# Optimization experiments

Measured on AMD Instinct MI355X. Metric: run time of the kernel, lower is better.

## Reference

```python
import jax, jax.numpy as jnp
import numpy as np

TWO_PI = 2.0 * np.pi
EPS = 1e-6

# mixture packed layout along last axis (7): [weight, px, py, cxx, cxy, cyx, cyy]

def unpack(m):
    w = m[..., 0]
    p = m[..., 1:3]
    C = m[..., 3:7].reshape(m.shape[:-1] + (2, 2))
    return w, p, C

def pack(w, p, C):
    return jnp.concatenate([w[..., None], p, C.reshape(C.shape[:-2] + (4,))], axis=-1)

def det2(C):
    return C[..., 0, 0] * C[..., 1, 1] - C[..., 0, 1] * C[..., 1, 0]

def inv2(C):
    d = det2(C)[..., None, None]
    adj = jnp.stack([
        jnp.stack([C[..., 1, 1], -C[..., 0, 1]], axis=-1),
        jnp.stack([-C[..., 1, 0], C[..., 0, 0]], axis=-1)], axis=-2)
    return adj / d

def component_integrals(w, C):
    # integral of an amplitude-parameterized 2D gaussian: w * 2*pi * sqrt(det C)
    return w * TWO_PI * jnp.sqrt(jnp.maximum(det2(C), EPS))

def gm_convolve(data, kernel):
    # data [B,Li,Nd,7], kernel [Lo,Li,Nk,7] -> [B,Lo,Li*Nd*Nk,7]
    wd, pd, Cd = unpack(data)
    wk, pk, Ck = unpack(kernel)
    dd = det2(Cd)[:, None, :, :, None]              # [B,1,Li,Nd,1]
    dk = det2(Ck)[None, :, :, None, :]              # [1,Lo,Li,1,Nk]
    Cs = Cd[:, None, :, :, None, :, :] + Ck[None, :, :, None, :, :, :]  # [B,Lo,Li,Nd,Nk,2,2]
    ps = pd[:, None, :, :, None, :] + pk[None, :, :, None, :, :]        # [B,Lo,Li,Nd,Nk,2]
    # amplitude of convolved gaussian so that integrals multiply
    ws = (wd[:, None, :, :, None] * wk[None, :, :, None, :]
          * TWO_PI * jnp.sqrt(dd * dk / jnp.maximum(det2(Cs), EPS)))
    m = pack(ws, ps, Cs)
    B, Lo = m.shape[0], m.shape[1]
    return m.reshape(B, Lo, -1, 7)

def eval_at_centers(w, p, C):
    # value of the whole mixture at each component center; [.., N]
    Ci = inv2(C)                                        # [..,N,2,2]
    diff = p[..., :, None, :] - p[..., None, :, :]      # [..,K,N,2]
    md = jnp.einsum('...kni,...nij,...knj->...kn', diff, Ci, diff)
    return jnp.einsum('...n,...kn->...k', w, jnp.exp(-0.5 * md))

def relu_fit(m, bias, n_out):
    # fitting-based ReLU: rescale each component so the mixture matches
    # relu(m(x)+b) at the centers, then keep the n_out largest components
    w, p, C = unpack(m)
    v = eval_at_centers(w, p, C) + bias[None, :, None]  # [B,L,N]
    scale = jax.nn.relu(v) / (jnp.abs(v) + EPS)
    w2 = w * scale
    _, idx = jax.lax.top_k(jnp.abs(w2), n_out)          # [B,L,n_out]
    w_s = jnp.take_along_axis(w2, idx, axis=-1)
    p_s = jnp.take_along_axis(p, jnp.broadcast_to(idx[..., None], idx.shape + (2,)), axis=-2)
    Cf = C.reshape(C.shape[:-2] + (4,))
    C_s = jnp.take_along_axis(Cf, jnp.broadcast_to(idx[..., None], idx.shape + (4,)), axis=-2)
    return pack(w_s, p_s, C_s.reshape(C_s.shape[:-1] + (2, 2)))

def batchnorm(m, per_gaussian):
    w, p, C = unpack(m)
    tot = jnp.sum(jnp.abs(component_integrals(w, C)), axis=-1, keepdims=True)  # [B,L,1]
    if not per_gaussian:
        tot = jnp.mean(tot, axis=0, keepdims=True)      # batch statistic per channel
    return pack(w / (tot + EPS), p, C)

def integrate(m):
    w, _, C = unpack(m)
    return jnp.sum(component_integrals(w, C), axis=-1)  # [B,L]

def forward(in_x, kernel1, kernel2, kernel3, bias1, bias2, bias3):
    x = batchnorm(in_x, per_gaussian=True)   # bn0
    x = gm_convolve(x, kernel1)              # [B,5,320,7]
    x = relu_fit(x, bias1, 25)
    x = batchnorm(x, per_gaussian=False)
    x = gm_convolve(x, kernel2)              # [B,6,625,7]
    x = relu_fit(x, bias2, 12)
    x = batchnorm(x, per_gaussian=False)
    x = gm_convolve(x, kernel3)              # [B,10,360,7]
    x = relu_fit(x, bias3, 5)
    x = batchnorm(x, per_gaussian=False)
    out = jax.nn.log_softmax(integrate(x), axis=1)
    return out.reshape(-1, 10)

def _make_kernel(key, lo, li, nk, weight_sd, position_range, covariance_range):
    kw, kp = jax.random.split(key)
    w = jax.random.normal(kw, (lo, li, nk)) * weight_sd
    p = jax.random.uniform(kp, (lo, li, nk, 2), minval=-position_range, maxval=position_range)
    C = jnp.broadcast_to(covariance_range * jnp.eye(2), (lo, li, nk, 2, 2))
    return pack(w, p, C).astype(jnp.float32)

def setup_inputs() -> dict:
    key = jax.random.key(0)
    k = jax.random.split(key, 8)
    B, NIN, NK = 32, 64, 5
    w = jax.random.uniform(k[0], (B, 1, NIN), minval=0.05, maxval=1.0)
    p = jax.random.uniform(k[1], (B, 1, NIN, 2), minval=-14.0, maxval=14.0)
    cdiag = jax.random.uniform(k[2], (B, 1, NIN, 2), minval=0.5, maxval=2.0)
    C = jnp.zeros((B, 1, NIN, 2, 2)).at[..., 0, 0].set(cdiag[..., 0]).at[..., 1, 1].set(cdiag[..., 1])
    in_x = pack(w, p, C).astype(jnp.float32)
    return {
        'in_x': in_x,
        'kernel1': _make_kernel(k[3], 5, 1, NK, 0.4, 2.0, 0.5),
        'kernel2': _make_kernel(k[4], 6, 5, NK, 0.04, 4.0, 2.0),
        'kernel3': _make_kernel(k[5], 10, 6, NK, 0.025, 8.0, 4.0),
        'bias1': jnp.zeros((5,), jnp.float32),
        'bias2': jnp.zeros((6,), jnp.float32),
        'bias3': jnp.zeros((10,), jnp.float32),
    }

def reference(in_x, kernel1, kernel2, kernel3, bias1, bias2, bias3):
    return forward(in_x, kernel1, kernel2, kernel3, bias1, bias2, bias3)
```

## Files before the change

### kernel.cpp

```cpp
#include <hip/hip_runtime.h>

#define TWO_PI_F 6.283185307179586f
#define EPS_F 1e-6f
#define LOG2E_F 1.4426950408889634f
#define BATCH 32

#if __has_builtin(__builtin_amdgcn_exp2f)
#define EXP2F(x) __builtin_amdgcn_exp2f(x)
#else
#define EXP2F(x) exp2f(x)
#endif

typedef float v2f __attribute__((ext_vector_type(2)));

__device__ __forceinline__ float sane(float x) {
    return ((__float_as_uint(x) & 0x7f800000u) == 0x7f800000u) ? 0.f : x;
}

__global__ __launch_bounds__(1024) void layer_unified(
    const float* __restrict__ in_x,
    const float* __restrict__ prev_sel,
    const float* __restrict__ prev_tot,
    const float* __restrict__ kern,
    const float* __restrict__ bias,
    float* __restrict__ out_sel,
    float* __restrict__ out_tot,
    const int LO, const int LI, const int ND, const int NK,
    const int NCOMP, const int KOUT,
    const int TPGL,
    const int G, const int CHUNK, const int CHUNKP,
    const int KUSE, const int first)
{
    constexpr int KP = 5, NT = 1024, NPAIR = 2;
    constexpr int M_NCOMP = 625, M_NCOMP4 = 628, M_NPADT = 8*80 + 4;
    constexpr int M_ACC   = 5120;
    struct StageT {
        float4 d_c[125];
        float4 k_c[25];
        float  d_w[125], d_px[125], d_py[125];
        float  k_w[25],  k_px[25],  k_py[25];
    };
    constexpr size_t ACCB = (size_t)M_ACC * sizeof(float);
    constexpr size_t UB   = sizeof(StageT) > ACCB ? sizeof(StageT) : ACCB;
    __shared__ __align__(16) unsigned char u_smem[UB];
    StageT& st    = *reinterpret_cast<StageT*>(u_smem);
    float* accbuf = reinterpret_cast<float*>(u_smem);

    __shared__ float2 cPos[M_NCOMP];
    __shared__ float4 nP[M_NPADT];
    __shared__ float4 nQ[M_NPADT];
    __shared__ float4 cC[M_NCOMP];
    __shared__ float  w2s[M_NCOMP];
    __shared__ __align__(16) float a2s[M_NCOMP4];
    __shared__ __align__(16) float scr[64];
    __shared__ float  selint[32];
    __shared__ float  dscale[8];
    __shared__ float  ptot[BATCH*5];

    const int b   = blockIdx.x / LO;
    const int lo  = blockIdx.x - b*LO;
    const int tid = threadIdx.x;
    const int tpg = 1 << TPGL;
    const int g   = tid >> TPGL;
    const int kt  = tid & (tpg - 1);
    const bool active = (kt < KUSE);
    const int NQn = (NCOMP + 3) >> 2;
    const int NCOMP4 = NQn << 2;
    const int NPADT = G*CHUNKP + 4;

    if (first) {
        if (tid < ND) {
            const float* s = in_x + (size_t)(b*ND + tid)*7;
            const float w  = sane(s[0]);
            const float c0 = sane(s[3]), c1 = sane(s[4]), c2 = sane(s[5]), c3 = sane(s[6]);
            st.d_w[tid] = w; st.d_px[tid] = sane(s[1]); st.d_py[tid] = sane(s[2]);
            st.d_c[tid] = make_float4(c0, c1, c2, c3);
            const float det = c0*c3 - c1*c2;
            scr[tid] = sane(fabsf(w) * TWO_PI_F * sqrtf(fmaxf(det, EPS_F)));
        }
        __syncthreads();
        if (tid == 0) {
            float s = 0.f;
            const float4* s4 = (const float4*)scr;
            const int nq = ND >> 2;
            for (int i = 0; i < nq; ++i) {
                const float4 v = s4[i];
                s += v.x; s += v.y; s += v.z; s += v.w;
            }
            dscale[0] = 1.f / (s + EPS_F);
        }
        __syncthreads();
        if (tid < ND) st.d_w[tid] = sane(st.d_w[tid] * dscale[0]);
    } else {
        for (int i = tid; i < BATCH*LI; i += NT) ptot[i] = prev_tot[i];
        __syncthreads();
        if (tid < LI) {
            float s = 0.f;
            #pragma unroll 1
            for (int bb = 0; bb < BATCH; ++bb) s += ptot[bb*LI + tid];
            dscale[tid] = 1.f / (s / (float)BATCH + EPS_F);
        }
        __syncthreads();
        if (tid < LI*ND) {
            const int li = tid / ND;
            const float* s = prev_sel + (size_t)(b*LI*ND + tid)*7;
            st.d_w[tid]  = sane(s[0] * dscale[li]);
            st.d_px[tid] = s[1]; st.d_py[tid] = s[2];
            st.d_c[tid]  = make_float4(s[3], s[4], s[5], s[6]);
        }
    }
    if (tid < LI*NK) {
        const float* s = kern + (size_t)(lo*LI*NK + tid)*7;
        st.k_w[tid]  = sane(s[0]);
        st.k_px[tid] = sane(s[1]); st.k_py[tid] = sane(s[2]);
        st.k_c[tid]  = make_float4(sane(s[3]), sane(s[4]), sane(s[5]), sane(s[6]));
    }
    for (int r = tid; r < NPADT; r += NT) {
        const int gg = r / CHUNKP;
        const int ss = r - gg*CHUNKP;
        const bool valid = (gg < G) && (ss < CHUNK) && (gg*CHUNK + ss < NCOMP);
        if (!valid) {
            nP[r] = make_float4(0.f, 0.f, 0.f, 0.f);
            nQ[r] = make_float4(0.f, 0.f, 0.f, 0.f);
        }
    }
    __syncthreads();

    if (tid < NCOMP) {
        const int li = tid / (ND*NK);
        const int r  = tid - li*(ND*NK);
        const int nd = r / NK, nk = r - (r/NK)*NK;
        const int di = li*ND + nd, ki = li*NK + nk;
        const float4 dc = st.d_c[di], kc = st.k_c[ki];
        const float c0 = dc.x + kc.x, c1 = dc.y + kc.y, c2 = dc.z + kc.z, c3 = dc.w + kc.w;
        const float dd = dc.x*dc.w - dc.y*dc.z;
        const float dk = kc.x*kc.w - kc.y*kc.z;
        const float ds = c0*c3 - c1*c2;
        const float w  = sane(st.d_w[di]*st.k_w[ki]*TWO_PI_F*sqrtf(fmaxf(dd*dk, 0.f) / fmaxf(ds, EPS_F)));
        const float px = sane(st.d_px[di] + st.k_px[ki]);
        const float py = sane(st.d_py[di] + st.k_py[ki]);
        const float inv = -0.5f * LOG2E_F / ds;
        const float a   = sane(c3*inv);
        const float bb  = sane(-(c1 + c2)*inv);
        const float cc  = sane(c0*inv);
        const float dd2 = sane(-(2.f*a*px + bb*py));
        const float ee  = sane(-(2.f*cc*py + bb*px));
        const float ff  = sane((a*px + bb*py)*px + cc*py*py);
        const int grp = tid / CHUNK;
        const int row = grp*CHUNKP + (tid - grp*CHUNK);
        cPos[tid] = make_float2(px, py);
        nP[row]   = make_float4(a, bb, cc, dd2);
        nQ[row]   = make_float4(ee, ff, w, 0.f);
        cC[tid]   = make_float4(sane(c0), sane(c1), sane(c2), sane(c3));
    }
    __syncthreads();

    v2f kxP[NPAIR], kyP[NPAIR], kx2P[NPAIR], ky2P[NPAIR], kxyP[NPAIR], accP[NPAIR];
    float kxS = 0.f, kyS = 0.f, kx2S = 0.f, ky2S = 0.f, kxyS = 0.f, accS = 0.f;
    #pragma unroll
    for (int p = 0; p < NPAIR; ++p) {
        float x0 = 0.f, y0 = 0.f, x1 = 0.f, y1 = 0.f;
        if (active) {
            const float2 p0 = cPos[kt + (2*p    )*KUSE];
            const float2 p1 = cPos[kt + (2*p + 1)*KUSE];
            x0 = p0.x; y0 = p0.y; x1 = p1.x; y1 = p1.y;
        }
        v2f kx; kx.x = x0; kx.y = x1;
        v2f ky; ky.x = y0; ky.y = y1;
        kxP[p] = kx; kyP[p] = ky;
        kx2P[p] = kx*kx; ky2P[p] = ky*ky; kxyP[p] = kx*ky;
        v2f z; z.x = 0.f; z.y = 0.f; accP[p] = z;
    }
    {
        if (active) { const float2 pz = cPos[kt + (KP-1)*KUSE]; kxS = pz.x; kyS = pz.y; }
        kx2S = kxS*kxS; ky2S = kyS*kyS; kxyS = kxS*kyS;
    }
    {
        const float4* __restrict__ bP = &nP[g*CHUNKP];
        const float4* __restrict__ bQ = &nQ[g*CHUNKP];
        float4 P0 = bP[0], Q0 = bQ[0];
        float4 P1 = bP[1], Q1 = bQ[1];
        float4 P2 = bP[2], Q2 = bQ[2];
        float4 P3 = bP[3], Q3 = bQ[3];
        int nr = 4;
        const int quads = CHUNKP >> 2;

#define PHB_STEP(PP,QQ)                                                       \
        {   const float4 Pn_ = bP[nr], Qn_ = bQ[nr]; ++nr;                    \
            v2f Pa; Pa.x = PP.x; Pa.y = PP.x;                                 \
            v2f Pb; Pb.x = PP.y; Pb.y = PP.y;                                 \
            v2f Pc; Pc.x = PP.z; Pc.y = PP.z;                                 \
            v2f Pd; Pd.x = PP.w; Pd.y = PP.w;                                 \
            v2f Qe; Qe.x = QQ.x; Qe.y = QQ.x;                                 \
            v2f Qf; Qf.x = QQ.y; Qf.y = QQ.y;                                 \
            v2f Qw; Qw.x = QQ.z; Qw.y = QQ.z;                                 \
            _Pragma("unroll")                                                 \
            for (int p = 0; p < NPAIR; ++p) {                                 \
                const v2f md = __builtin_elementwise_fma(Pa, kx2P[p],         \
                               __builtin_elementwise_fma(Pb, kxyP[p],         \
                               __builtin_elementwise_fma(Pc, ky2P[p],         \
                               __builtin_elementwise_fma(Pd, kxP[p],          \
                               __builtin_elementwise_fma(Qe, kyP[p], Qf)))));  \
                v2f ex; ex.x = EXP2F(md.x); ex.y = EXP2F(md.y);               \
                accP[p] = __builtin_elementwise_fma(Qw, ex, accP[p]);         \
            }                                                                 \
            {                                                                 \
                const float md = fmaf(PP.x, kx2S,                             \
                                 fmaf(PP.y, kxyS,                             \
                                 fmaf(PP.z, ky2S,                             \
                                 fmaf(PP.w, kxS,                              \
                                 fmaf(QQ.x, kyS, QQ.y)))));                   \
                accS = fmaf(QQ.z, EXP2F(md), accS);                           \
            }                                                                 \
            PP = Pn_; QQ = Qn_; }

        #pragma unroll 1
        for (int i4 = 0; i4 < quads; ++i4) {
            PHB_STEP(P0, Q0)
            PHB_STEP(P1, Q1)
            PHB_STEP(P2, Q2)
            PHB_STEP(P3, Q3)
        }
#undef PHB_STEP
    }
    float acc[KP];
    #pragma unroll
    for (int p = 0; p < NPAIR; ++p) { acc[2*p] = accP[p].x; acc[2*p+1] = accP[p].y; }
    acc[KP-1] = accS;

    if (active) {
        #pragma unroll
        for (int j = 0; j < KP; ++j) accbuf[(g*tpg + kt)*KP + j] = acc[j];
    }
    __syncthreads();

    const float bi = bias[lo];
    if (tid < NCOMP) {
        const int j2  = tid / KUSE;
        const int kt2 = tid - j2*KUSE;
        float s = accbuf[kt2*KP + j2];
        #pragma unroll 1
        for (int g2 = 1; g2 < G; ++g2) s += accbuf[(g2*tpg + kt2)*KP + j2];
        const float v  = s + bi;
        const float sc = fmaxf(v, 0.f) / (fabsf(v) + EPS_F);
        const int grp = tid / CHUNK;
        const int row = grp*CHUNKP + (tid - grp*CHUNK);
        const float ww = sane(nQ[row].z * sc);
        w2s[tid] = ww;
        a2s[tid] = fabsf(ww);
    }
    for (int i = NCOMP + tid - (tid < NCOMP ? tid : tid); false;) {}
    if (tid >= NCOMP && tid < NCOMP4) a2s[tid] = -1.f;
    __syncthreads();

    const int CQ = (NQn + G - 1) / G;
    int rank[KP];
    float myv[KP];
    #pragma unroll
    for (int j = 0; j < KP; ++j) rank[j] = 0;
    if (active) {
        #pragma unroll
        for (int j = 0; j < KP; ++j) myv[j] = a2s[kt + j*KUSE];
        const int q0 = g*CQ;
        const int q1 = (q0 + CQ < NQn) ? (q0 + CQ) : NQn;
        #pragma unroll 1
        for (int q = q0; q < q1; ++q) {
            const float4 v4 = ((const float4*)a2s)[q];
            #pragma unroll
            for (int c = 0; c < 4; ++c) {
                const float vj = (c == 0) ? v4.x : (c == 1) ? v4.y : (c == 2) ? v4.z : v4.w;
                const int   jj = 4*q + c;
                #pragma unroll
                for (int j = 0; j < KP; ++j) {
                    const int myk = kt + j*KUSE;
                    rank[j] += (vj > myv[j] || (vj == myv[j] && jj < myk)) ? 1 : 0;
                }
            }
        }
        #pragma unroll
        for (int j = 0; j < KP; ++j) accbuf[(g*tpg + kt)*KP + j] = (float)rank[j];
    }
    __syncthreads();

    if (tid < NCOMP) {
        const int j2  = tid / KUSE;
        const int kt2 = tid - j2*KUSE;
        int r = 0;
        #pragma unroll 1
        for (int g2 = 0; g2 < G; ++g2) r += (int)accbuf[(g2*tpg + kt2)*KP + j2];
        if (r < KOUT) {
            const float2 p = cPos[tid];
            const float4 c = cC[tid];
            const float ww = w2s[tid];
            float* dst = out_sel + (size_t)((b*LO + lo)*KOUT + r)*7;
            dst[0] = ww; dst[1] = p.x; dst[2] = p.y;
            dst[3] = c.x; dst[4] = c.y; dst[5] = c.z; dst[6] = c.w;
            const float det = c.x*c.w - c.y*c.z;
            selint[r] = sane(fabsf(ww) * TWO_PI_F * sqrtf(fmaxf(det, EPS_F)));
        }
    }
    __syncthreads();
    if (tid == 0) {
        float s = 0.f;
        #pragma unroll 1
        for (int i = 0; i < KOUT; ++i) s += selint[i];
        out_tot[b*LO + lo] = s;
    }
}

template<int LO, int LI, int ND, int NK, int NCOMP, int KOUT,
         int KP, int TPG, int G, bool FIRST>
__global__ __launch_bounds__(TPG*G) void layer_kernel(
    const float* __restrict__ in_x,
    const float* __restrict__ prev_sel,
    const float* __restrict__ prev_tot,
    const float* __restrict__ kern,
    const float* __restrict__ bias,
    float* __restrict__ out_sel,
    float* __restrict__ out_tot)
{
    constexpr int KUSE   = NCOMP / KP;
    static_assert(KUSE * KP == NCOMP, "exact k tiling required");
    constexpr int NT     = TPG * G;
    static_assert(NT >= NCOMP, "one k per thread in reduce/select phases");
    constexpr int CHUNK  = (NCOMP + G - 1) / G;
    constexpr int NPADT  = G*CHUNK + 4;
    constexpr int NCOMP4 = (NCOMP + 3) & ~3;
    constexpr int NQn    = NCOMP4 / 4;
    constexpr int NPAIR  = KP / 2;
    constexpr int PPAD   = NPAIR > 0 ? NPAIR : 1;
    constexpr bool ODD   = (KP & 1) != 0;

    const int b   = blockIdx.x / LO;
    const int lo  = blockIdx.x % LO;
    const int tid = threadIdx.x;
    const int g   = tid / TPG;
    const int kt  = tid % TPG;
    const bool active = (kt < KUSE);

    struct StageT {
        float4 d_c[LI*ND];
        float4 k_c[LI*NK];
        float  d_w[LI*ND], d_px[LI*ND], d_py[LI*ND];
        float  k_w[LI*NK], k_px[LI*NK], k_py[LI*NK];
    };
    constexpr size_t ACCB = (size_t)G*TPG*KP * sizeof(float);
    constexpr size_t UB   = sizeof(StageT) > ACCB ? sizeof(StageT) : ACCB;
    __shared__ __align__(16) unsigned char u_smem[UB];
    StageT& st    = *reinterpret_cast<StageT*>(u_smem);
    float* accbuf = reinterpret_cast<float*>(u_smem);

    __shared__ float2 cPos[NCOMP];
    __shared__ float4 nP[NPADT];
    __shared__ float4 nQ[NPADT];
    __shared__ float4 cC[NCOMP];
    __shared__ float  w2s[NCOMP];
    __shared__ __align__(16) float a2s[NCOMP4];
    __shared__ __align__(16) float scr[64];
    __shared__ float  selint[32];
    __shared__ float  dscale[LI];
    __shared__ float  ptot[FIRST ? 1 : BATCH*LI];

    if constexpr (FIRST) {
        if (tid < ND) {
            const float* s = in_x + (size_t)(b*ND + tid)*7;
            const float w  = sane(s[0]);
            const float c0 = sane(s[3]), c1 = sane(s[4]), c2 = sane(s[5]), c3 = sane(s[6]);
            st.d_w[tid] = w; st.d_px[tid] = sane(s[1]); st.d_py[tid] = sane(s[2]);
            st.d_c[tid] = make_float4(c0, c1, c2, c3);
            const float det = c0*c3 - c1*c2;
            scr[tid] = sane(fabsf(w) * TWO_PI_F * sqrtf(fmaxf(det, EPS_F)));
        }
        __syncthreads();
        if (tid == 0) {
            float s = 0.f;
            const float4* s4 = (const float4*)scr;
            for (int i = 0; i < 16; ++i) {
                const float4 v = s4[i];
                s += v.x; s += v.y; s += v.z; s += v.w;
            }
            dscale[0] = 1.f / (s + EPS_F);
        }
        __syncthreads();
        if (tid < ND) st.d_w[tid] = sane(st.d_w[tid] * dscale[0]);
    } else {
        for (int i = tid; i < BATCH*LI; i += NT) ptot[i] = prev_tot[i];
        __syncthreads();
        if (tid < LI) {
            float s = 0.f;
            #pragma unroll 1
            for (int bb = 0; bb < BATCH; ++bb) s += ptot[bb*LI + tid];
            dscale[tid] = 1.f / (s / (float)BATCH + EPS_F);
        }
        __syncthreads();
        if (tid < LI*ND) {
            const int li = tid / ND;
            const float* s = prev_sel + (size_t)(b*LI*ND + tid)*7;
            st.d_w[tid]  = sane(s[0] * dscale[li]);
            st.d_px[tid] = s[1]; st.d_py[tid] = s[2];
            st.d_c[tid]  = make_float4(s[3], s[4], s[5], s[6]);
        }
    }
    if (tid < LI*NK) {
        const float* s = kern + (size_t)(lo*LI*NK + tid)*7;
        st.k_w[tid]  = sane(s[0]);
        st.k_px[tid] = sane(s[1]); st.k_py[tid] = sane(s[2]);
        st.k_c[tid]  = make_float4(sane(s[3]), sane(s[4]), sane(s[5]), sane(s[6]));
    }
    __syncthreads();

    if (tid < NCOMP) {
        const int li = tid / (ND*NK);
        const int r  = tid % (ND*NK);
        const int nd = r / NK, nk = r % NK;
        const int di = li*ND + nd, ki = li*NK + nk;
        const float4 dc = st.d_c[di], kc = st.k_c[ki];
        const float c0 = dc.x + kc.x, c1 = dc.y + kc.y, c2 = dc.z + kc.z, c3 = dc.w + kc.w;
        const float dd = dc.x*dc.w - dc.y*dc.z;
        const float dk = kc.x*kc.w - kc.y*kc.z;
        const float ds = c0*c3 - c1*c2;
        const float w  = sane(st.d_w[di]*st.k_w[ki]*TWO_PI_F*sqrtf(fmaxf(dd*dk, 0.f) / fmaxf(ds, EPS_F)));
        const float px = sane(st.d_px[di] + st.k_px[ki]);
        const float py = sane(st.d_py[di] + st.k_py[ki]);
        const float inv = -0.5f * LOG2E_F / ds;
        const float a   = sane(c3*inv);
        const float bb  = sane(-(c1 + c2)*inv);
        const float cc  = sane(c0*inv);
        const float dd2 = sane(-(2.f*a*px + bb*py));
        const float ee  = sane(-(2.f*cc*py + bb*px));
        const float ff  = sane((a*px + bb*py)*px + cc*py*py);
        cPos[tid] = make_float2(px, py);
        nP[tid]   = make_float4(a, bb, cc, dd2);
        nQ[tid]   = make_float4(ee, ff, w, 0.f);
        cC[tid]   = make_float4(sane(c0), sane(c1), sane(c2), sane(c3));
    }
    for (int i = NCOMP + tid; i < NPADT; i += NT) {
        nP[i] = make_float4(0.f, 0.f, 0.f, 0.f);
        nQ[i] = make_float4(0.f, 0.f, 0.f, 0.f);
    }
    __syncthreads();

    v2f kxP[PPAD], kyP[PPAD], kx2P[PPAD], ky2P[PPAD], kxyP[PPAD], accP[PPAD];
    float kxS = 0.f, kyS = 0.f, kx2S = 0.f, ky2S = 0.f, kxyS = 0.f, accS = 0.f;
    #pragma unroll
    for (int p = 0; p < NPAIR; ++p) {
        float x0 = 0.f, y0 = 0.f, x1 = 0.f, y1 = 0.f;
        if (active) {
            const float2 p0 = cPos[kt + (2*p    )*KUSE];
            const float2 p1 = cPos[kt + (2*p + 1)*KUSE];
            x0 = p0.x; y0 = p0.y; x1 = p1.x; y1 = p1.y;
        }
        v2f kx; kx.x = x0; kx.y = x1;
        v2f ky; ky.x = y0; ky.y = y1;
        kxP[p] = kx; kyP[p] = ky;
        kx2P[p] = kx*kx; ky2P[p] = ky*ky; kxyP[p] = kx*ky;
        v2f z; z.x = 0.f; z.y = 0.f; accP[p] = z;
    }
    if constexpr (ODD) {
        if (active) { const float2 pz = cPos[kt + (KP-1)*KUSE]; kxS = pz.x; kyS = pz.y; }
        kx2S = kxS*kxS; ky2S = kyS*kyS; kxyS = kxS*kyS;
    }
    {
        const int n0 = g*CHUNK;
        const float4* __restrict__ bP = &nP[n0];
        const float4* __restrict__ bQ = &nQ[n0];
        float4 P0 = bP[0], Q0 = bQ[0];
        float4 P1 = bP[1], Q1 = bQ[1];
        float4 P2 = bP[2], Q2 = bQ[2];
        float4 P3 = bP[3], Q3 = bQ[3];
        int nr = 4;

#define PHB_STEP(PP,QQ)                                                       \
        {   const float4 Pn_ = bP[nr], Qn_ = bQ[nr]; ++nr;                    \
            v2f Pa; Pa.x = PP.x; Pa.y = PP.x;                                 \
            v2f Pb; Pb.x = PP.y; Pb.y = PP.y;                                 \
            v2f Pc; Pc.x = PP.z; Pc.y = PP.z;                                 \
            v2f Pd; Pd.x = PP.w; Pd.y = PP.w;                                 \
            v2f Qe; Qe.x = QQ.x; Qe.y = QQ.x;                                 \
            v2f Qf; Qf.x = QQ.y; Qf.y = QQ.y;                                 \
            v2f Qw; Qw.x = QQ.z; Qw.y = QQ.z;                                 \
            _Pragma("unroll")                                                 \
            for (int p = 0; p < NPAIR; ++p) {                                 \
                const v2f md = __builtin_elementwise_fma(Pa, kx2P[p],         \
                               __builtin_elementwise_fma(Pb, kxyP[p],         \
                               __builtin_elementwise_fma(Pc, ky2P[p],         \
                               __builtin_elementwise_fma(Pd, kxP[p],          \
                               __builtin_elementwise_fma(Qe, kyP[p], Qf)))));  \
                v2f ex; ex.x = EXP2F(md.x); ex.y = EXP2F(md.y);               \
                accP[p] = __builtin_elementwise_fma(Qw, ex, accP[p]);         \
            }                                                                 \
            if constexpr (ODD) {                                              \
                const float md = fmaf(PP.x, kx2S,                             \
                                 fmaf(PP.y, kxyS,                             \
                                 fmaf(PP.z, ky2S,                             \
                                 fmaf(PP.w, kxS,                              \
                                 fmaf(QQ.x, kyS, QQ.y)))));                   \
                accS = fmaf(QQ.z, EXP2F(md), accS);                           \
            }                                                                 \
            PP = Pn_; QQ = Qn_; }

        #pragma unroll 1
        for (int i4 = 0; i4 < CHUNK/4; ++i4) {
            PHB_STEP(P0, Q0)
            PHB_STEP(P1, Q1)
            PHB_STEP(P2, Q2)
            PHB_STEP(P3, Q3)
        }
        if constexpr ((CHUNK % 4) >= 1) PHB_STEP(P0, Q0)
        if constexpr ((CHUNK % 4) >= 2) PHB_STEP(P1, Q1)
        if constexpr ((CHUNK % 4) >= 3) PHB_STEP(P2, Q2)
#undef PHB_STEP
    }
    float acc[KP];
    #pragma unroll
    for (int p = 0; p < NPAIR; ++p) { acc[2*p] = accP[p].x; acc[2*p+1] = accP[p].y; }
    if constexpr (ODD) acc[KP-1] = accS;

    if (active) {
        #pragma unroll
        for (int j = 0; j < KP; ++j) accbuf[(g*TPG + kt)*KP + j] = acc[j];
    }
    __syncthreads();

    const float bi = bias[lo];
    if (tid < NCOMP) {
        const int kt2 = tid % KUSE;
        const int j2  = tid / KUSE;
        float s = accbuf[(kt2)*KP + j2];
        #pragma unroll
        for (int g2 = 1; g2 < G; ++g2) s += accbuf[(g2*TPG + kt2)*KP + j2];
        const float v  = s + bi;
        const float sc = fmaxf(v, 0.f) / (fabsf(v) + EPS_F);
        const float ww = sane(nQ[tid].z * sc);
        w2s[tid] = ww;
        a2s[tid] = fabsf(ww);
    }
    if constexpr (NCOMP4 > NCOMP) {
        if (tid >= NCOMP && tid < NCOMP4) a2s[tid] = -1.f;
    }
    __syncthreads();

    constexpr int CQ = (NQn + G - 1) / G;
    int rank[KP];
    float myv[KP];
    #pragma unroll
    for (int j = 0; j < KP; ++j) rank[j] = 0;
    if (active) {
        #pragma unroll
        for (int j = 0; j < KP; ++j) myv[j] = a2s[kt + j*KUSE];
        const int q0 = g*CQ;
        const int q1 = (q0 + CQ < NQn) ? (q0 + CQ) : NQn;
        for (int q = q0; q < q1; ++q) {
            const float4 v4 = ((const float4*)a2s)[q];
            #pragma unroll
            for (int c = 0; c < 4; ++c) {
                const float vj = (c == 0) ? v4.x : (c == 1) ? v4.y : (c == 2) ? v4.z : v4.w;
                const int   jj = 4*q + c;
                #pragma unroll
                for (int j = 0; j < KP; ++j) {
                    const int myk = kt + j*KUSE;
                    rank[j] += (vj > myv[j] || (vj == myv[j] && jj < myk)) ? 1 : 0;
                }
            }
        }
        #pragma unroll
        for (int j = 0; j < KP; ++j) accbuf[(g*TPG + kt)*KP + j] = (float)rank[j];
    }
    __syncthreads();

    if (tid < NCOMP) {
        const int kt2 = tid % KUSE;
// ... 26 lines not shown
    float* __restrict__ out)
{
    const int b = blockIdx.x;
    const int tid = threadIdx.x;
    __shared__ float scale3[10], integ[10], red2[2];
    if (tid < 10) {
        float s = 0.f;
        for (int bb = 0; bb < BATCH; ++bb) s += tot3[bb*10 + tid];
        scale3[tid] = 1.f / (s / (float)BATCH + EPS_F);
    }
    __syncthreads();
    if (tid < 10) {
        float s = 0.f;
        const float* base = sel3 + (size_t)((b*10 + tid)*5)*7;
        for (int kk = 0; kk < 5; ++kk) {
            const float* c = base + kk*7;
            const float det = c[3]*c[6] - c[4]*c[5];
            s += c[0] * scale3[tid] * TWO_PI_F * sqrtf(fmaxf(det, EPS_F));
        }
        integ[tid] = sane(s);
    }
    __syncthreads();
    if (tid == 0) {
        float m = -1e30f;
        for (int l = 0; l < 10; ++l) m = fmaxf(m, integ[l]);
        float ss = 0.f;
        for (int l = 0; l < 10; ++l) ss += __expf(integ[l] - m);
        red2[0] = m; red2[1] = logf(ss);
    }
    __syncthreads();
    if (tid < 10) out[b*10 + tid] = integ[tid] - red2[0] - red2[1];
}

extern "C" void kernel_launch(void* const* d_in, const int* in_sizes, int n_in,
                              void* d_out, int out_size, void* d_ws, size_t ws_size,
                              hipStream_t stream)
{
    const float* in_x = (const float*)d_in[0];
    const float* k1   = (const float*)d_in[1];
    const float* k2   = (const float*)d_in[2];
    const float* k3   = (const float*)d_in[3];
    const float* b1   = (const float*)d_in[4];
    const float* b2   = (const float*)d_in[5];
    const float* b3   = (const float*)d_in[6];
    float* out = (float*)d_out;

    float* ws = (float*)d_ws;
    float* sel1 = ws;
    float* tot1 = ws + 28000;
    float* sel2 = ws + 28160;
    float* tot2 = ws + 44288;
    float* sel3 = ws + 44480;
    float* tot3 = ws + 55680;

    layer_unified<<<BATCH*5, 1024, 0, stream>>>(
        in_x, nullptr, nullptr, k1, b1, sel1, tot1,
        5, 1, 64, 5, 320, 25, 6, 16, 20, 20, 64, 1);
    layer_unified<<<BATCH*6, 1024, 0, stream>>>(
        nullptr, sel1, tot1, k2, b2, sel2, tot2,
        6, 5, 25, 5, 625, 12, 7, 8, 79, 80, 125, 0);
    layer_kernel<10, 6, 12, 5, 360, 5, 6, 64, 12, false><<<BATCH*10, 768, 0, stream>>>(
        nullptr, sel2, tot2, k3, b3, sel3, tot3);
    final_kernel<<<BATCH, 64, 0, stream>>>(sel3, tot3, out);
}
```

Measured before the change: 148.3 us.

## Split layers 1-2 into separate evaluation and selection kernels via global scratch

```diff
diff --git a/kernel.cpp b/kernel.cpp
--- a/kernel.cpp
+++ b/kernel.cpp
@@ -17,347 +17,43 @@
     return ((__float_as_uint(x) & 0x7f800000u) == 0x7f800000u) ? 0.f : x;
 }
 
-__global__ __launch_bounds__(1024) void layer_unified(
+
+template<int LO, int LI, int ND, int NK, int NCOMP,
+         int KP, int TPG, int G, bool FIRST>
+__global__ __launch_bounds__(TPG*G) void layer_partA(
     const float* __restrict__ in_x,
     const float* __restrict__ prev_sel,
     const float* __restrict__ prev_tot,
     const float* __restrict__ kern,
-    const float* __restrict__ bias,
-    float* __restrict__ out_sel,
-    float* __restrict__ out_tot,
-    const int LO, const int LI, const int ND, const int NK,
-    const int NCOMP, const int KOUT,
-    const int TPGL,
-    const int G, const int CHUNK, const int CHUNKP,
-    const int KUSE, const int first)
-{
-    constexpr int KP = 5, NT = 1024, NPAIR = 2;
-    constexpr int M_NCOMP = 625, M_NCOMP4 = 628, M_NPADT = 8*80 + 4;
-    constexpr int M_ACC   = 5120;
-    struct StageT {
-        float4 d_c[125];
-        float4 k_c[25];
-        float  d_w[125], d_px[125], d_py[125];
-        float  k_w[25],  k_px[25],  k_py[25];
-    };
-    constexpr size_t ACCB = (size_t)M_ACC * sizeof(float);
-    constexpr size_t UB   = sizeof(StageT) > ACCB ? sizeof(StageT) : ACCB;
-    __shared__ __align__(16) unsigned char u_smem[UB];
-    StageT& st    = *reinterpret_cast<StageT*>(u_smem);
-    float* accbuf = reinterpret_cast<float*>(u_smem);
-
-    __shared__ float2 cPos[M_NCOMP];
-    __shared__ float4 nP[M_NPADT];
-    __shared__ float4 nQ[M_NPADT];
-    __shared__ float4 cC[M_NCOMP];
-    __shared__ float  w2s[M_NCOMP];
-    __shared__ __align__(16) float a2s[M_NCOMP4];
-    __shared__ __align__(16) float scr[64];
-    __shared__ float  selint[32];
-    __shared__ float  dscale[8];
-    __shared__ float  ptot[BATCH*5];
-
-    const int b   = blockIdx.x / LO;
-    const int lo  = blockIdx.x - b*LO;
-    const int tid = threadIdx.x;
-    const int tpg = 1 << TPGL;
-    const int g   = tid >> TPGL;
-    const int kt  = tid & (tpg - 1);
-    const bool active = (kt < KUSE);
-    const int NQn = (NCOMP + 3) >> 2;
-    const int NCOMP4 = NQn << 2;
-    const int NPADT = G*CHUNKP + 4;
-
-    if (first) {
-        if (tid < ND) {
-            const float* s = in_x + (size_t)(b*ND + tid)*7;
-            const float w  = sane(s[0]);
-            const float c0 = sane(s[3]), c1 = sane(s[4]), c2 = sane(s[5]), c3 = sane(s[6]);
-            st.d_w[tid] = w; st.d_px[tid] = sane(s[1]); st.d_py[tid] = sane(s[2]);
-            st.d_c[tid] = make_float4(c0, c1, c2, c3);
-            const float det = c0*c3 - c1*c2;
-            scr[tid] = sane(fabsf(w) * TWO_PI_F * sqrtf(fmaxf(det, EPS_F)));
-        }
-        __syncthreads();
-        if (tid == 0) {
-            float s = 0.f;
-            const float4* s4 = (const float4*)scr;
-            const int nq = ND >> 2;
-            for (int i = 0; i < nq; ++i) {
-                const float4 v = s4[i];
-                s += v.x; s += v.y; s += v.z; s += v.w;
-            }
-            dscale[0] = 1.f / (s + EPS_F);
-        }
-        __syncthreads();
-        if (tid < ND) st.d_w[tid] = sane(st.d_w[tid] * dscale[0]);
-    } else {
-        for (int i = tid; i < BATCH*LI; i += NT) ptot[i] = prev_tot[i];
-        __syncthreads();
-        if (tid < LI) {
-            float s = 0.f;
-            #pragma unroll 1
-            for (int bb = 0; bb < BATCH; ++bb) s += ptot[bb*LI + tid];
-            dscale[tid] = 1.f / (s / (float)BATCH + EPS_F);
-        }
-        __syncthreads();
-        if (tid < LI*ND) {
-            const int li = tid / ND;
-            const float* s = prev_sel + (size_t)(b*LI*ND + tid)*7;
-            st.d_w[tid]  = sane(s[0] * dscale[li]);
-            st.d_px[tid] = s[1]; st.d_py[tid] = s[2];
-            st.d_c[tid]  = make_float4(s[3], s[4], s[5], s[6]);
-        }
-    }
-    if (tid < LI*NK) {
-        const float* s = kern + (size_t)(lo*LI*NK + tid)*7;
-        st.k_w[tid]  = sane(s[0]);
-        st.k_px[tid] = sane(s[1]); st.k_py[tid] = sane(s[2]);
-        st.k_c[tid]  = make_float4(sane(s[3]), sane(s[4]), sane(s[5]), sane(s[6]));
-    }
-    for (int r = tid; r < NPADT; r += NT) {
-        const int gg = r / CHUNKP;
-        const int ss = r - gg*CHUNKP;
-        const bool valid = (gg < G) && (ss < CHUNK) && (gg*CHUNK + ss < NCOMP);
-        if (!valid) {
-            nP[r] = make_float4(0.f, 0.f, 0.f, 0.f);
-            nQ[r] = make_float4(0.f, 0.f, 0.f, 0.f);
-        }
-    }
-    __syncthreads();
-
-    if (tid < NCOMP) {
-        const int li = tid / (ND*NK);
-        const int r  = tid - li*(ND*NK);
-        const int nd = r / NK, nk = r - (r/NK)*NK;
-        const int di = li*ND + nd, ki = li*NK + nk;
-        const float4 dc = st.d_c[di], kc = st.k_c[ki];
-        const float c0 = dc.x + kc.x, c1 = dc.y + kc.y, c2 = dc.z + kc.z, c3 = dc.w + kc.w;
-        const float dd = dc.x*dc.w - dc.y*dc.z;
-        const float dk = kc.x*kc.w - kc.y*kc.z;
-        const float ds = c0*c3 - c1*c2;
-        const float w  = sane(st.d_w[di]*st.k_w[ki]*TWO_PI_F*sqrtf(fmaxf(dd*dk, 0.f) / fmaxf(ds, EPS_F)));
-        const float px = sane(st.d_px[di] + st.k_px[ki]);
-        const float py = sane(st.d_py[di] + st.k_py[ki]);
-        const float inv = -0.5f * LOG2E_F / ds;
-        const float a   = sane(c3*inv);
-        const float bb  = sane(-(c1 + c2)*inv);
-        const float cc  = sane(c0*inv);
-        const float dd2 = sane(-(2.f*a*px + bb*py));
-        const float ee  = sane(-(2.f*cc*py + bb*px));
-        const float ff  = sane((a*px + bb*py)*px + cc*py*py);
-        const int grp = tid / CHUNK;
-        const int row = grp*CHUNKP + (tid - grp*CHUNK);
-        cPos[tid] = make_float2(px, py);
-        nP[row]   = make_float4(a, bb, cc, dd2);
-        nQ[row]   = make_float4(ee, ff, w, 0.f);
-        cC[tid]   = make_float4(sane(c0), sane(c1), sane(c2), sane(c3));
-    }
-    __syncthreads();
-
-    v2f kxP[NPAIR], kyP[NPAIR], kx2P[NPAIR], ky2P[NPAIR], kxyP[NPAIR], accP[NPAIR];
-    float kxS = 0.f, kyS = 0.f, kx2S = 0.f, ky2S = 0.f, kxyS = 0.f, accS = 0.f;
-    #pragma unroll
-    for (int p = 0; p < NPAIR; ++p) {
-        float x0 = 0.f, y0 = 0.f, x1 = 0.f, y1 = 0.f;
-        if (active) {
-            const float2 p0 = cPos[kt + (2*p    )*KUSE];
-            const float2 p1 = cPos[kt + (2*p + 1)*KUSE];
-            x0 = p0.x; y0 = p0.y; x1 = p1.x; y1 = p1.y;
-        }
-        v2f kx; kx.x = x0; kx.y = x1;
-        v2f ky; ky.x = y0; ky.y = y1;
-        kxP[p] = kx; kyP[p] = ky;
-        kx2P[p] = kx*kx; ky2P[p] = ky*ky; kxyP[p] = kx*ky;
-        v2f z; z.x = 0.f; z.y = 0.f; accP[p] = z;
-    }
-    {
-        if (active) { const float2 pz = cPos[kt + (KP-1)*KUSE]; kxS = pz.x; kyS = pz.y; }
-        kx2S = kxS*kxS; ky2S = kyS*kyS; kxyS = kxS*kyS;
-    }
-    {
-        const float4* __restrict__ bP = &nP[g*CHUNKP];
-        const float4* __restrict__ bQ = &nQ[g*CHUNKP];
-        float4 P0 = bP[0], Q0 = bQ[0];
-        float4 P1 = bP[1], Q1 = bQ[1];
-        float4 P2 = bP[2], Q2 = bQ[2];
-        float4 P3 = bP[3], Q3 = bQ[3];
-        int nr = 4;
-        const int quads = CHUNKP >> 2;
-
-#define PHB_STEP(PP,QQ)                                                       \
-        {   const float4 Pn_ = bP[nr], Qn_ = bQ[nr]; ++nr;                    \
-            v2f Pa; Pa.x = PP.x; Pa.y = PP.x;                                 \
-            v2f Pb; Pb.x = PP.y; Pb.y = PP.y;                                 \
-            v2f Pc; Pc.x = PP.z; Pc.y = PP.z;                                 \
-            v2f Pd; Pd.x = PP.w; Pd.y = PP.w;                                 \
-            v2f Qe; Qe.x = QQ.x; Qe.y = QQ.x;                                 \
-            v2f Qf; Qf.x = QQ.y; Qf.y = QQ.y;                                 \
-            v2f Qw; Qw.x = QQ.z; Qw.y = QQ.z;                                 \
-            _Pragma("unroll")                                                 \
-            for (int p = 0; p < NPAIR; ++p) {                                 \
-                const v2f md = __builtin_elementwise_fma(Pa, kx2P[p],         \
-                               __builtin_elementwise_fma(Pb, kxyP[p],         \
-                               __builtin_elementwise_fma(Pc, ky2P[p],         \
-                               __builtin_elementwise_fma(Pd, kxP[p],          \
-                               __builtin_elementwise_fma(Qe, kyP[p], Qf)))));  \
-                v2f ex; ex.x = EXP2F(md.x); ex.y = EXP2F(md.y);               \
-                accP[p] = __builtin_elementwise_fma(Qw, ex, accP[p]);         \
-            }                                                                 \
-            {                                                                 \
-                const float md = fmaf(PP.x, kx2S,                             \
-                                 fmaf(PP.y, kxyS,                             \
-                                 fmaf(PP.z, ky2S,                             \
-                                 fmaf(PP.w, kxS,                              \
-                                 fmaf(QQ.x, kyS, QQ.y)))));                   \
-                accS = fmaf(QQ.z, EXP2F(md), accS);                           \
-            }                                                                 \
-            PP = Pn_; QQ = Qn_; }
-
-        #pragma unroll 1
-        for (int i4 = 0; i4 < quads; ++i4) {
-            PHB_STEP(P0, Q0)
-            PHB_STEP(P1, Q1)
-            PHB_STEP(P2, Q2)
-            PHB_STEP(P3, Q3)
-        }
-#undef PHB_STEP
-    }
-    float acc[KP];
-    #pragma unroll
-    for (int p = 0; p < NPAIR; ++p) { acc[2*p] = accP[p].x; acc[2*p+1] = accP[p].y; }
-    acc[KP-1] = accS;
-
-    if (active) {
-        #pragma unroll
-        for (int j = 0; j < KP; ++j) accbuf[(g*tpg + kt)*KP + j] = acc[j];
-    }
-    __syncthreads();
-
-    const float bi = bias[lo];
-    if (tid < NCOMP) {
-        const int j2  = tid / KUSE;
-        const int kt2 = tid - j2*KUSE;
-        float s = accbuf[kt2*KP + j2];
-        #pragma unroll 1
-        for (int g2 = 1; g2 < G; ++g2) s += accbuf[(g2*tpg + kt2)*KP + j2];
-        const float v  = s + bi;
-        const float sc = fmaxf(v, 0.f) / (fabsf(v) + EPS_F);
-        const int grp = tid / CHUNK;
-        const int row = grp*CHUNKP + (tid - grp*CHUNK);
-        const float ww = sane(nQ[row].z * sc);
-        w2s[tid] = ww;
-        a2s[tid] = fabsf(ww);
-    }
-    for (int i = NCOMP + tid - (tid < NCOMP ? tid : tid); false;) {}
-    if (tid >= NCOMP && tid < NCOMP4) a2s[tid] = -1.f;
-    __syncthreads();
-
-    const int CQ = (NQn + G - 1) / G;
-    int rank[KP];
-    float myv[KP];
-    #pragma unroll
-    for (int j = 0; j < KP; ++j) rank[j] = 0;
-    if (active) {
-        #pragma unroll
-        for (int j = 0; j < KP; ++j) myv[j] = a2s[kt + j*KUSE];
-        const int q0 = g*CQ;
-        const int q1 = (q0 + CQ < NQn) ? (q0 + CQ) : NQn;
-        #pragma unroll 1
-        for (int q = q0; q < q1; ++q) {
-            const float4 v4 = ((const float4*)a2s)[q];
-            #pragma unroll
-            for (int c = 0; c < 4; ++c) {
-                const float vj = (c == 0) ? v4.x : (c == 1) ? v4.y : (c == 2) ? v4.z : v4.w;
-                const int   jj = 4*q + c;
-                #pragma unroll
-                for (int j = 0; j < KP; ++j) {
-                    const int myk = kt + j*KUSE;
-                    rank[j] += (vj > myv[j] || (vj == myv[j] && jj < myk)) ? 1 : 0;
-                }
-            }
-        }
-        #pragma unroll
-        for (int j = 0; j < KP; ++j) accbuf[(g*tpg + kt)*KP + j] = (float)rank[j];
-    }
-    __syncthreads();
-
-    if (tid < NCOMP) {
-        const int j2  = tid / KUSE;
-        const int kt2 = tid - j2*KUSE;
-        int r = 0;
-        #pragma unroll 1
-        for (int g2 = 0; g2 < G; ++g2) r += (int)accbuf[(g2*tpg + kt2)*KP + j2];
-        if (r < KOUT) {
-            const float2 p = cPos[tid];
-            const float4 c = cC[tid];
-            const float ww = w2s[tid];
-            float* dst = out_sel + (size_t)((b*LO + lo)*KOUT + r)*7;
-            dst[0] = ww; dst[1] = p.x; dst[2] = p.y;
-            dst[3] = c.x; dst[4] = c.y; dst[5] = c.z; dst[6] = c.w;
-            const float det = c.x*c.w - c.y*c.z;
-            selint[r] = sane(fabsf(ww) * TWO_PI_F * sqrtf(fmaxf(det, EPS_F)));
-        }
-    }
-    __syncthreads();
-    if (tid == 0) {
-        float s = 0.f;
-        #pragma unroll 1
-        for (int i = 0; i < KOUT; ++i) s += selint[i];
-        out_tot[b*LO + lo] = s;
-    }
-}
-
-template<int LO, int LI, int ND, int NK, int NCOMP, int KOUT,
-         int KP, int TPG, int G, bool FIRST>
-__global__ __launch_bounds__(TPG*G) void layer_kernel(
-    const float* __restrict__ in_x,
-    const float* __restrict__ prev_sel,
-    const float* __restrict__ prev_tot,
-    const float* __restrict__ kern,
-    const float* __restrict__ bias,
-    float* __restrict__ out_sel,
-    float* __restrict__ out_tot)
+    float* __restrict__ comp7,
+    float* __restrict__ gpart)
 {
     constexpr int KUSE   = NCOMP / KP;
     static_assert(KUSE * KP == NCOMP, "exact k tiling required");
     constexpr int NT     = TPG * G;
-    static_assert(NT >= NCOMP, "one k per thread in reduce/select phases");
     constexpr int CHUNK  = (NCOMP + G - 1) / G;
     constexpr int NPADT  = G*CHUNK + 4;
-    constexpr int NCOMP4 = (NCOMP + 3) & ~3;
-    constexpr int NQn    = NCOMP4 / 4;
     constexpr int NPAIR  = KP / 2;
-    constexpr int PPAD   = NPAIR > 0 ? NPAIR : 1;
     constexpr bool ODD   = (KP & 1) != 0;
 
     const int b   = blockIdx.x / LO;
     const int lo  = blockIdx.x % LO;
+    const int unit = b*LO + lo;
     const int tid = threadIdx.x;
     const int g   = tid / TPG;
     const int kt  = tid % TPG;
     const bool active = (kt < KUSE);
 
-    struct StageT {
+    __shared__ struct {
         float4 d_c[LI*ND];
         float4 k_c[LI*NK];
         float  d_w[LI*ND], d_px[LI*ND], d_py[LI*ND];
         float  k_w[LI*NK], k_px[LI*NK], k_py[LI*NK];
-    };
-    constexpr size_t ACCB = (size_t)G*TPG*KP * sizeof(float);
-    constexpr size_t UB   = sizeof(StageT) > ACCB ? sizeof(StageT) : ACCB;
-    __shared__ __align__(16) unsigned char u_smem[UB];
-    StageT& st    = *reinterpret_cast<StageT*>(u_smem);
-    float* accbuf = reinterpret_cast<float*>(u_smem);
-
+    } st;
     __shared__ float2 cPos[NCOMP];
     __shared__ float4 nP[NPADT];
     __shared__ float4 nQ[NPADT];
-    __shared__ float4 cC[NCOMP];
-    __shared__ float  w2s[NCOMP];
-    __shared__ __align__(16) float a2s[NCOMP4];
     __shared__ __align__(16) float scr[64];
-    __shared__ float  selint[32];
     __shared__ float  dscale[LI];
     __shared__ float  ptot[FIRST ? 1 : BATCH*LI];
 
@@ -432,7 +128,9 @@
         cPos[tid] = make_float2(px, py);
         nP[tid]   = make_float4(a, bb, cc, dd2);
         nQ[tid]   = make_float4(ee, ff, w, 0.f);
-        cC[tid]   = make_float4(sane(c0), sane(c1), sane(c2), sane(c3));
+        float* c7 = comp7 + ((size_t)unit*NCOMP + tid)*8;
+        *(float4*)c7       = make_float4(w, px, py, sane(c0));
+        *(float4*)(c7 + 4) = make_float4(sane(c1), sane(c2), sane(c3), 0.f);
     }
     for (int i = NCOMP + tid; i < NPADT; i += NT) {
         nP[i] = make_float4(0.f, 0.f, 0.f, 0.f);
@@ -440,7 +138,8 @@
     }
     __syncthreads();
 
-    v2f kxP[PPAD], kyP[PPAD], kx2P[PPAD], ky2P[PPAD], kxyP[PPAD], accP[PPAD];
+    v2f kxP[NPAIR ? NPAIR : 1], kyP[NPAIR ? NPAIR : 1], kx2P[NPAIR ? NPAIR : 1],
+        ky2P[NPAIR ? NPAIR : 1], kxyP[NPAIR ? NPAIR : 1], accP[NPAIR ? NPAIR : 1];
     float kxS = 0.f, kyS = 0.f, kx2S = 0.f, ky2S = 0.f, kxyS = 0.f, accS = 0.f;
     #pragma unroll
     for (int p = 0; p < NPAIR; ++p) {
@@ -517,6 +216,319 @@
     if constexpr (ODD) acc[KP-1] = accS;
 
     if (active) {
+        float* gp = gpart + ((size_t)unit*G + g)*(TPG*KP);
+        #pragma unroll
+        for (int j = 0; j < KP; ++j) gp[kt*KP + j] = acc[j];
+    }
+}
+
+template<int LO, int NCOMP, int KOUT, int KP, int TPG, int G>
+__global__ __launch_bounds__(TPG*G) void layer_partB(
+    const float* __restrict__ comp7,
+    const float* __restrict__ gpart,
+    const float* __restrict__ bias,
+    float* __restrict__ out_sel,
+    float* __restrict__ out_tot)
+{
+    constexpr int KUSE   = NCOMP / KP;
+    constexpr int NT     = TPG * G;
+    static_assert(NT >= NCOMP, "one k per thread");
+    constexpr int NCOMP4 = (NCOMP + 3) & ~3;
+    constexpr int NQn    = NCOMP4 / 4;
+    constexpr int CQ     = (NQn + G - 1) / G;
+
+    const int unit = blockIdx.x;
+    const int lo   = unit % LO;
+    const int tid  = threadIdx.x;
+    const int g    = tid / TPG;
+    const int kt   = tid % TPG;
+    const bool active = (kt < KUSE);
+
+    __shared__ float accbuf[G*TPG*KP];
+    __shared__ float w2s[NCOMP];
+    __shared__ __align__(16) float a2s[NCOMP4];
+    __shared__ float selint[32];
+
+    const float bi = bias[lo];
+    const float* gb = gpart + (size_t)unit*G*(TPG*KP);
+    if (tid < NCOMP) {
+        const int j2  = tid / KUSE;
+        const int kt2 = tid - j2*KUSE;
+        float s = gb[kt2*KP + j2];
+        #pragma unroll 1
+        for (int g2 = 1; g2 < G; ++g2) s += gb[(size_t)g2*(TPG*KP) + kt2*KP + j2];
+        const float v  = s + bi;
+        const float sc = fmaxf(v, 0.f) / (fabsf(v) + EPS_F);
+        const float ww = sane(comp7[((size_t)unit*NCOMP + tid)*8] * sc);
+        w2s[tid] = ww;
+        a2s[tid] = fabsf(ww);
+    }
+    if (tid >= NCOMP && tid < NCOMP4) a2s[tid] = -1.f;
+    __syncthreads();
+
+    int rank[KP];
+    float myv[KP];
+    #pragma unroll
+    for (int j = 0; j < KP; ++j) rank[j] = 0;
+    if (active) {
+        #pragma unroll
+        for (int j = 0; j < KP; ++j) myv[j] = a2s[kt + j*KUSE];
+        const int q0 = g*CQ;
+        const int q1 = (q0 + CQ < NQn) ? (q0 + CQ) : NQn;
+        #pragma unroll 1
+        for (int q = q0; q < q1; ++q) {
+            const float4 v4 = ((const float4*)a2s)[q];
+            #pragma unroll
+            for (int c = 0; c < 4; ++c) {
+                const float vj = (c == 0) ? v4.x : (c == 1) ? v4.y : (c == 2) ? v4.z : v4.w;
+                const int   jj = 4*q + c;
+                #pragma unroll
+                for (int j = 0; j < KP; ++j) {
+                    const int myk = kt + j*KUSE;
+                    rank[j] += (vj > myv[j] || (vj == myv[j] && jj < myk)) ? 1 : 0;
+                }
+            }
+        }
+        #pragma unroll
+        for (int j = 0; j < KP; ++j) accbuf[(g*TPG + kt)*KP + j] = (float)rank[j];
+    }
+    __syncthreads();
+
+    if (tid < NCOMP) {
+        const int j2  = tid / KUSE;
+        const int kt2 = tid - j2*KUSE;
+        int r = 0;
+        #pragma unroll 1
+        for (int g2 = 0; g2 < G; ++g2) r += (int)accbuf[(g2*TPG + kt2)*KP + j2];
+        if (r < KOUT) {
+            const float4 c0 = *(const float4*)&comp7[((size_t)unit*NCOMP + tid)*8];
+            const float4 c1 = *(const float4*)&comp7[((size_t)unit*NCOMP + tid)*8 + 4];
+            const float ww = w2s[tid];
+            float* dst = out_sel + (size_t)(unit*KOUT + r)*7;
+            dst[0] = ww; dst[1] = c0.y; dst[2] = c0.z;
+            dst[3] = c0.w; dst[4] = c1.x; dst[5] = c1.y; dst[6] = c1.z;
+            const float det = c0.w*c1.z - c1.x*c1.y;
+            selint[r] = sane(fabsf(ww) * TWO_PI_F * sqrtf(fmaxf(det, EPS_F)));
+        }
+    }
+    __syncthreads();
+    if (tid == 0) {
+        float s = 0.f;
+        #pragma unroll 1
+        for (int i = 0; i < KOUT; ++i) s += selint[i];
+        out_tot[unit] = s;
+    }
+}
+
+template<int LO, int LI, int ND, int NK, int NCOMP, int KOUT,
+         int KP, int TPG, int G, bool FIRST>
+__global__ __launch_bounds__(TPG*G) void layer_kernel(
+    const float* __restrict__ in_x,
+    const float* __restrict__ prev_sel,
+    const float* __restrict__ prev_tot,
+    const float* __restrict__ kern,
+    const float* __restrict__ bias,
+    float* __restrict__ out_sel,
+    float* __restrict__ out_tot)
+{
+    constexpr int KUSE   = NCOMP / KP;
+    static_assert(KUSE * KP == NCOMP, "exact k tiling required");
+    constexpr int NT     = TPG * G;
+    static_assert(NT >= NCOMP, "one k per thread in reduce/select phases");
+    constexpr int CHUNK  = (NCOMP + G - 1) / G;
+    constexpr int NPADT  = G*CHUNK + 4;
+    constexpr int NCOMP4 = (NCOMP + 3) & ~3;
+    constexpr int NQn    = NCOMP4 / 4;
+    constexpr int NPAIR  = KP / 2;
+    constexpr int PPAD   = NPAIR > 0 ? NPAIR : 1;
+    constexpr bool ODD   = (KP & 1) != 0;
+
+    const int b   = blockIdx.x / LO;
+    const int lo  = blockIdx.x % LO;
+    const int tid = threadIdx.x;
+    const int g   = tid / TPG;
+    const int kt  = tid % TPG;
+    const bool active = (kt < KUSE);
+
+    struct StageT {
+        float4 d_c[LI*ND];
+        float4 k_c[LI*NK];
+        float  d_w[LI*ND], d_px[LI*ND], d_py[LI*ND];
+        float  k_w[LI*NK], k_px[LI*NK], k_py[LI*NK];
+    };
+    constexpr size_t ACCB = (size_t)G*TPG*KP * sizeof(float);
+    constexpr size_t UB   = sizeof(StageT) > ACCB ? sizeof(StageT) : ACCB;
+    __shared__ __align__(16) unsigned char u_smem[UB];
+    StageT& st    = *reinterpret_cast<StageT*>(u_smem);
+    float* accbuf = reinterpret_cast<float*>(u_smem);
+
+    __shared__ float2 cPos[NCOMP];
+    __shared__ float4 nP[NPADT];
+    __shared__ float4 nQ[NPADT];
+    __shared__ float4 cC[NCOMP];
+    __shared__ float  w2s[NCOMP];
+    __shared__ __align__(16) float a2s[NCOMP4];
+    __shared__ __align__(16) float scr[64];
+    __shared__ float  selint[32];
+    __shared__ float  dscale[LI];
+    __shared__ float  ptot[FIRST ? 1 : BATCH*LI];
+
+    if constexpr (FIRST) {
+        if (tid < ND) {
+            const float* s = in_x + (size_t)(b*ND + tid)*7;
+            const float w  = sane(s[0]);
+            const float c0 = sane(s[3]), c1 = sane(s[4]), c2 = sane(s[5]), c3 = sane(s[6]);
+            st.d_w[tid] = w; st.d_px[tid] = sane(s[1]); st.d_py[tid] = sane(s[2]);
+            st.d_c[tid] = make_float4(c0, c1, c2, c3);
+            const float det = c0*c3 - c1*c2;
+            scr[tid] = sane(fabsf(w) * TWO_PI_F * sqrtf(fmaxf(det, EPS_F)));
+        }
+        __syncthreads();
+        if (tid == 0) {
+            float s = 0.f;
+            const float4* s4 = (const float4*)scr;
+            for (int i = 0; i < 16; ++i) {
+                const float4 v = s4[i];
+                s += v.x; s += v.y; s += v.z; s += v.w;
+            }
+            dscale[0] = 1.f / (s + EPS_F);
+        }
+        __syncthreads();
+        if (tid < ND) st.d_w[tid] = sane(st.d_w[tid] * dscale[0]);
+    } else {
+        for (int i = tid; i < BATCH*LI; i += NT) ptot[i] = prev_tot[i];
+        __syncthreads();
+        if (tid < LI) {
+            float s = 0.f;
+            #pragma unroll 1
+            for (int bb = 0; bb < BATCH; ++bb) s += ptot[bb*LI + tid];
+            dscale[tid] = 1.f / (s / (float)BATCH + EPS_F);
+        }
+        __syncthreads();
+        if (tid < LI*ND) {
+            const int li = tid / ND;
+            const float* s = prev_sel + (size_t)(b*LI*ND + tid)*7;
+            st.d_w[tid]  = sane(s[0] * dscale[li]);
+            st.d_px[tid] = s[1]; st.d_py[tid] = s[2];
+            st.d_c[tid]  = make_float4(s[3], s[4], s[5], s[6]);
+        }
+    }
+    if (tid < LI*NK) {
+        const float* s = kern + (size_t)(lo*LI*NK + tid)*7;
+        st.k_w[tid]  = sane(s[0]);
+        st.k_px[tid] = sane(s[1]); st.k_py[tid] = sane(s[2]);
+        st.k_c[tid]  = make_float4(sane(s[3]), sane(s[4]), sane(s[5]), sane(s[6]));
+    }
+    __syncthreads();
+
+    if (tid < NCOMP) {
+        const int li = tid / (ND*NK);
+        const int r  = tid % (ND*NK);
+        const int nd = r / NK, nk = r % NK;
+        const int di = li*ND + nd, ki = li*NK + nk;
+        const float4 dc = st.d_c[di], kc = st.k_c[ki];
+        const float c0 = dc.x + kc.x, c1 = dc.y + kc.y, c2 = dc.z + kc.z, c3 = dc.w + kc.w;
+        const float dd = dc.x*dc.w - dc.y*dc.z;
+        const float dk = kc.x*kc.w - kc.y*kc.z;
+        const float ds = c0*c3 - c1*c2;
+        const float w  = sane(st.d_w[di]*st.k_w[ki]*TWO_PI_F*sqrtf(fmaxf(dd*dk, 0.f) / fmaxf(ds, EPS_F)));
+        const float px = sane(st.d_px[di] + st.k_px[ki]);
+        const float py = sane(st.d_py[di] + st.k_py[ki]);
+        const float inv = -0.5f * LOG2E_F / ds;
+        const float a   = sane(c3*inv);
+        const float bb  = sane(-(c1 + c2)*inv);
+        const float cc  = sane(c0*inv);
+        const float dd2 = sane(-(2.f*a*px + bb*py));
+        const float ee  = sane(-(2.f*cc*py + bb*px));
+        const float ff  = sane((a*px + bb*py)*px + cc*py*py);
+        cPos[tid] = make_float2(px, py);
+        nP[tid]   = make_float4(a, bb, cc, dd2);
+        nQ[tid]   = make_float4(ee, ff, w, 0.f);
+        cC[tid]   = make_float4(sane(c0), sane(c1), sane(c2), sane(c3));
+    }
+    for (int i = NCOMP + tid; i < NPADT; i += NT) {
+        nP[i] = make_float4(0.f, 0.f, 0.f, 0.f);
+        nQ[i] = make_float4(0.f, 0.f, 0.f, 0.f);
+    }
+    __syncthreads();
+
+    v2f kxP[PPAD], kyP[PPAD], kx2P[PPAD], ky2P[PPAD], kxyP[PPAD], accP[PPAD];
+    float kxS = 0.f, kyS = 0.f, kx2S = 0.f, ky2S = 0.f, kxyS = 0.f, accS = 0.f;
+    #pragma unroll
+    for (int p = 0; p < NPAIR; ++p) {
+        float x0 = 0.f, y0 = 0.f, x1 = 0.f, y1 = 0.f;
+        if (active) {
+            const float2 p0 = cPos[kt + (2*p    )*KUSE];
+            const float2 p1 = cPos[kt + (2*p + 1)*KUSE];
+            x0 = p0.x; y0 = p0.y; x1 = p1.x; y1 = p1.y;
+        }
+        v2f kx; kx.x = x0; kx.y = x1;
+        v2f ky; ky.x = y0; ky.y = y1;
+        kxP[p] = kx; kyP[p] = ky;
+        kx2P[p] = kx*kx; ky2P[p] = ky*ky; kxyP[p] = kx*ky;
+        v2f z; z.x = 0.f; z.y = 0.f; accP[p] = z;
+    }
+    if constexpr (ODD) {
+        if (active) { const float2 pz = cPos[kt + (KP-1)*KUSE]; kxS = pz.x; kyS = pz.y; }
+        kx2S = kxS*kxS; ky2S = kyS*kyS; kxyS = kxS*kyS;
+    }
+    {
+        const int n0 = g*CHUNK;
+        const float4* __restrict__ bP = &nP[n0];
+        const float4* __restrict__ bQ = &nQ[n0];
+        float4 P0 = bP[0], Q0 = bQ[0];
+        float4 P1 = bP[1], Q1 = bQ[1];
+        float4 P2 = bP[2], Q2 = bQ[2];
+        float4 P3 = bP[3], Q3 = bQ[3];
+        int nr = 4;
+
+#define PHB_STEP(PP,QQ)                                                       \
+        {   const float4 Pn_ = bP[nr], Qn_ = bQ[nr]; ++nr;                    \
+            v2f Pa; Pa.x = PP.x; Pa.y = PP.x;                                 \
+            v2f Pb; Pb.x = PP.y; Pb.y = PP.y;                                 \
+            v2f Pc; Pc.x = PP.z; Pc.y = PP.z;                                 \
+            v2f Pd; Pd.x = PP.w; Pd.y = PP.w;                                 \
+            v2f Qe; Qe.x = QQ.x; Qe.y = QQ.x;                                 \
+            v2f Qf; Qf.x = QQ.y; Qf.y = QQ.y;                                 \
+            v2f Qw; Qw.x = QQ.z; Qw.y = QQ.z;                                 \
+            _Pragma("unroll")                                                 \
+            for (int p = 0; p < NPAIR; ++p) {                                 \
+                const v2f md = __builtin_elementwise_fma(Pa, kx2P[p],         \
+                               __builtin_elementwise_fma(Pb, kxyP[p],         \
+                               __builtin_elementwise_fma(Pc, ky2P[p],         \
+                               __builtin_elementwise_fma(Pd, kxP[p],          \
+                               __builtin_elementwise_fma(Qe, kyP[p], Qf)))));  \
+                v2f ex; ex.x = EXP2F(md.x); ex.y = EXP2F(md.y);               \
+                accP[p] = __builtin_elementwise_fma(Qw, ex, accP[p]);         \
+            }                                                                 \
+            if constexpr (ODD) {                                              \
+                const float md = fmaf(PP.x, kx2S,                             \
+                                 fmaf(PP.y, kxyS,                             \
+                                 fmaf(PP.z, ky2S,                             \
+                                 fmaf(PP.w, kxS,                              \
+                                 fmaf(QQ.x, kyS, QQ.y)))));                   \
+                accS = fmaf(QQ.z, EXP2F(md), accS);                           \
+            }                                                                 \
+            PP = Pn_; QQ = Qn_; }
+
+        #pragma unroll 1
+        for (int i4 = 0; i4 < CHUNK/4; ++i4) {
+            PHB_STEP(P0, Q0)
+            PHB_STEP(P1, Q1)
+            PHB_STEP(P2, Q2)
+            PHB_STEP(P3, Q3)
+        }
+        if constexpr ((CHUNK % 4) >= 1) PHB_STEP(P0, Q0)
+        if constexpr ((CHUNK % 4) >= 2) PHB_STEP(P1, Q1)
+        if constexpr ((CHUNK % 4) >= 3) PHB_STEP(P2, Q2)
+#undef PHB_STEP
+    }
+    float acc[KP];
+    #pragma unroll
+    for (int p = 0; p < NPAIR; ++p) { acc[2*p] = accP[p].x; acc[2*p+1] = accP[p].y; }
+    if constexpr (ODD) acc[KP-1] = accS;
+
+    if (active) {
         #pragma unroll
         for (int j = 0; j < KP; ++j) accbuf[(g*TPG + kt)*KP + j] = acc[j];
     }
@@ -649,13 +661,19 @@
     float* tot2 = ws + 44288;
     float* sel3 = ws + 44480;
     float* tot3 = ws + 55680;
-
-    layer_unified<<<BATCH*5, 1024, 0, stream>>>(
-        in_x, nullptr, nullptr, k1, b1, sel1, tot1,
-        5, 1, 64, 5, 320, 25, 6, 16, 20, 20, 64, 1);
-    layer_unified<<<BATCH*6, 1024, 0, stream>>>(
-        nullptr, sel1, tot1, k2, b2, sel2, tot2,
-        6, 5, 25, 5, 625, 12, 7, 8, 79, 80, 125, 0);
+    float* comp7_1 = ws + 56000;
+    float* gpart1  = ws + 465600;
+    float* comp7_2 = ws + 1284800;
+    float* gpart2  = ws + 2244800;
+
+    layer_partA<5, 1, 64, 5, 320, 5, 64, 16, true><<<BATCH*5, 1024, 0, stream>>>(
+        in_x, nullptr, nullptr, k1, comp7_1, gpart1);
+    layer_partB<5, 320, 25, 5, 64, 16><<<BATCH*5, 1024, 0, stream>>>(
+        comp7_1, gpart1, b1, sel1, tot1);
+    layer_partA<6, 5, 25, 5, 625, 5, 128, 8, false><<<BATCH*6, 1024, 0, stream>>>(
+        nullptr, sel1, tot1, k2, comp7_2, gpart2);
+    layer_partB<6, 625, 12, 5, 128, 8><<<BATCH*6, 1024, 0, stream>>>(
+        comp7_2, gpart2, b2, sel2, tot2);
     layer_kernel<10, 6, 12, 5, 360, 5, 6, 64, 12, false><<<BATCH*10, 768, 0, stream>>>(
         nullptr, sel2, tot2, k3, b3, sel3, tot3);
     final_kernel<<<BATCH, 64, 0, stream>>>(sel3, tot3, out);
```

After: 160.0 us. 7.9% more time.
